# Performance work log

Measured on AMD Instinct MI355X. Metric: run time of the kernel, lower is better.

Reference implementation:

```python
import jax, jax.numpy as jnp
import numpy as np

B, S, HID = 2, 1024, 1024
NH, CH, HD = 16, 32, 64          # standard heads, constitutional heads, head_dim
TRUST = 64


def setup_inputs() -> dict:
    key = jax.random.key(0)
    ks = jax.random.split(key, 16)
    g = lambda k, sh, sc: jax.random.normal(k, sh, dtype=jnp.float32) * sc
    w = 1.0 / np.sqrt(HID)
    inp = {
        'hidden_states': g(ks[0], (B, S, HID), 1.0),
        'attention_mask': g(ks[1], (B, 1, S, S), 1.0),
        'trust_scores': jax.random.uniform(ks[2], (B, TRUST), dtype=jnp.float32),
        'Wq': g(ks[3], (HID, HID), w), 'bq': jnp.zeros((HID,), jnp.float32),
        'Wk': g(ks[4], (HID, HID), w), 'bk': jnp.zeros((HID,), jnp.float32),
        'Wv': g(ks[5], (HID, HID), w), 'bv': jnp.zeros((HID,), jnp.float32),
        'Wcq': g(ks[6], (HID, CH * HD), w), 'bcq': jnp.zeros((CH * HD,), jnp.float32),
        'Wck': g(ks[7], (HID, CH * HD), w), 'bck': jnp.zeros((CH * HD,), jnp.float32),
        'Wcv': g(ks[8], (HID, CH * HD), w), 'bcv': jnp.zeros((CH * HD,), jnp.float32),
        'Wt': g(ks[9], (TRUST, NH), 1.0 / np.sqrt(TRUST)), 'bt': jnp.zeros((NH,), jnp.float32),
        'Wo': g(ks[10], (HID, HID), w), 'bo': jnp.zeros((HID,), jnp.float32),
    }
    return inp


def reference(hidden_states, attention_mask, trust_scores,
              Wq, bq, Wk, bk, Wv, bv,
              Wcq, bcq, Wck, bck, Wcv, bcv,
              Wt, bt, Wo, bo):
    x = hidden_states
    scale = 1.0 / np.sqrt(HD).astype(np.float32)

    # standard QKV -> [B, NH, S, HD]
    q = (x @ Wq + bq).reshape(B, S, NH, HD)
    k = (x @ Wk + bk).reshape(B, S, NH, HD)
    v = (x @ Wv + bv).reshape(B, S, NH, HD)
    scores = jnp.einsum('bqhd,bkhd->bhqk', q, k) * scale  # [B,NH,S,S]
    scores = scores + attention_mask                       # additive mask

    # constitutional QKV -> [B, CH, S, HD]
    cq = (x @ Wcq + bcq).reshape(B, S, CH, HD)
    ck = (x @ Wck + bck).reshape(B, S, CH, HD)
    const_scores = jnp.einsum('bqhd,bkhd->bhqk', cq, ck) * scale  # [B,CH,S,S]

    # trust weighting: [B,TRUST] -> [B,NH] broadcast over [S,S]
    tw = trust_scores @ Wt + bt
    scores = scores * tw[:, :, None, None]

    # combine: per-head scores + mean over constitutional heads
    combined = scores + jnp.mean(const_scores, axis=1, keepdims=True)
    probs = jax.nn.softmax(combined, axis=-1)  # dropout is identity in eval

    context = jnp.einsum('bhqk,bkhd->bqhd', probs, v).reshape(B, S, HID)
    output = context @ Wo + bo
    return output, probs


if __name__ == '__main__':
    out, probs = reference(**setup_inputs())
    print(out.shape, probs.shape)
```

## Files before the change

kernel.cpp:

```cpp
#include <hip/hip_runtime.h>


typedef __bf16 bf16x8 __attribute__((ext_vector_type(8)));
typedef __bf16 bf16x4 __attribute__((ext_vector_type(4)));
typedef short  s16x4  __attribute__((ext_vector_type(4)));
typedef float  f32x4  __attribute__((ext_vector_type(4)));

static constexpr int Sq  = 1024;
static constexpr int LDP = 7168;

#if defined(__has_builtin)
#  if __has_builtin(__builtin_amdgcn_mfma_f32_16x16x16bf16_1k)
#    define HAVE_MFMA16B 1
#  endif
#endif

__device__ __forceinline__ void mfma16(f32x4& c, bf16x4 a, bf16x4 b)
{
#ifdef HAVE_MFMA16B
    union { bf16x4 h; s16x4 s; } ua, ub;
    ua.h = a; ub.h = b;
    c = __builtin_amdgcn_mfma_f32_16x16x16bf16_1k(ua.s, ub.s, c, 0, 0, 0);
#else
    asm volatile("v_mfma_f32_16x16x16_bf16 %0, %1, %2, %0"
                 : "+v"(c) : "v"(a), "v"(b));
#endif
}

template<int ROWS>
__device__ __forceinline__ void stage_g(const __bf16* g, int ld, __bf16* s, int tid)
{
    constexpr int PER = (ROWS * 4) / 256;
    int w = tid >> 6, l = tid & 63;
#pragma unroll
    for (int i = 0; i < PER; i++) {
        int bc = w * 64 + i * 256;
        int chunk = bc + l;
        int row = chunk >> 2, part = (chunk & 3) * 8;
        const __bf16* gp = g + (size_t)row * ld + part;
        __bf16* sp = s + (size_t)bc * 8;
        __builtin_amdgcn_global_load_lds(
            (__attribute__((address_space(1))) void*)(gp),
            (__attribute__((address_space(3))) void*)(sp), 16, 0, 0);
    }
}

template<int BM, int BN, int EPI>
__global__ __launch_bounds__(256) void gemm_nt(
    const __bf16* __restrict__ A, int lda,
    const __bf16* __restrict__ B, int ldb,
    void* __restrict__ Cout, int ldc,
    const float* __restrict__ bias, int Ksz, float alpha)
{
    constexpr int WM = BM / 2, WN = BN / 2, FM = WM / 16, FN = WN / 16;
    __shared__ __bf16 As[BM][32];
    __shared__ __bf16 Bs[BN][32];
    int tid = threadIdx.x;
    int w = tid >> 6, l = tid & 63;
    int wr = w >> 1, wc = w & 1;
    int lr = l & 15, kp = (l >> 4) * 8;
    int bm = blockIdx.x * BM, bn = blockIdx.y * BN;
    int z = blockIdx.z;

    size_t zA = 0, zC = 0;
    if constexpr (EPI == 2) { zA = (size_t)z * 1024 * LDP; zC = (size_t)z * Sq * Sq; }

    f32x4 acc[FM][FN];
#pragma unroll
    for (int i = 0; i < FM; i++)
#pragma unroll
        for (int j = 0; j < FN; j++) acc[i][j] = (f32x4){0.f, 0.f, 0.f, 0.f};

    for (int k0 = 0; k0 < Ksz; k0 += 32) {
        stage_g<BM>(A + zA + (size_t)bm * lda + k0, lda, &As[0][0], tid);
        stage_g<BN>(B + zA + (size_t)bn * ldb + k0, ldb, &Bs[0][0], tid);
        __syncthreads();
        bf16x8 av[FM], bv[FN];
#pragma unroll
        for (int i = 0; i < FM; i++) av[i] = *(const bf16x8*)&As[wr * WM + i * 16 + lr][kp];
#pragma unroll
        for (int j = 0; j < FN; j++) bv[j] = *(const bf16x8*)&Bs[wc * WN + j * 16 + lr][kp];
#pragma unroll
        for (int i = 0; i < FM; i++)
#pragma unroll
            for (int j = 0; j < FN; j++)
                acc[i][j] = __builtin_amdgcn_mfma_f32_16x16x32_bf16(av[i], bv[j], acc[i][j], 0, 0, 0);
        __syncthreads();
    }

    int dr = (l >> 4) * 4, dc = l & 15;
#pragma unroll
    for (int i = 0; i < FM; i++)
#pragma unroll
        for (int j = 0; j < FN; j++)
#pragma unroll
            for (int t = 0; t < 4; t++) {
                int row = bm + wr * WM + i * 16 + dr + t;
                int col = bn + wc * WN + j * 16 + dc;
                float v = acc[i][j][t];
                size_t off = zC + (size_t)row * ldc + col;
                if constexpr (EPI == 0)      ((__bf16*)Cout)[off] = (__bf16)(v + bias[col]);
                else if constexpr (EPI == 1) ((float*)Cout)[off]  = v + bias[col];
                else                         ((float*)Cout)[off]  = v * alpha;
            }
}

__global__ __launch_bounds__(256, 2) void attn_fused(
    const __bf16* __restrict__ PROJ, const __bf16* __restrict__ Kp,
    const __bf16* __restrict__ Vp,
    const float* __restrict__ mask, const float* __restrict__ CM,
    const float* __restrict__ TW, float* __restrict__ probs,
    __bf16* __restrict__ CTXb)
{
    __shared__ float ctxred[4][64][36];
    __shared__ float red[32][4];

    int tid = threadIdx.x;
    int w = tid >> 6, l = tid & 63;
    int lr = l & 15, g = l >> 4, kp = g * 8;

    int bid = blockIdx.x;
    int low3 = bid & 7;
    int t6   = bid >> 3;
    int h    = t6 & 15;
    int g64  = (t6 >> 4) * 8 + low3;
    int b    = g64 >> 5;
    int bm   = (g64 & 31) * 32;
    int z    = b * 16 + h;

    const __bf16* Qg  = PROJ + (size_t)(b * 1024 + bm) * LDP + h * 64;
    const __bf16* Kzp = Kp + (size_t)z * 65536;
    const __bf16* Vzp = Vp + (size_t)z * 65536;

    bf16x8 qv[2][2];
#pragma unroll
    for (int i = 0; i < 2; i++)
#pragma unroll
        for (int kk = 0; kk < 2; kk++)
            qv[i][kk] = *(const bf16x8*)(Qg + (size_t)(i * 16 + lr) * LDP + kk * 32 + kp);

    f32x4 acc[2][16];
#pragma unroll
    for (int i = 0; i < 2; i++)
#pragma unroll
        for (int j = 0; j < 16; j++) acc[i][j] = (f32x4){0.f, 0.f, 0.f, 0.f};

#pragma unroll
    for (int j = 0; j < 16; j++) {
        int T = w * 16 + j;
        bf16x8 k0 = *(const bf16x8*)(Kzp + ((size_t)(T * 2 + 0) * 64 + l) * 8);
        bf16x8 k1 = *(const bf16x8*)(Kzp + ((size_t)(T * 2 + 1) * 64 + l) * 8);
#pragma unroll
        for (int i = 0; i < 2; i++) {
            acc[i][j] = __builtin_amdgcn_mfma_f32_16x16x32_bf16(k0, qv[i][0], acc[i][j], 0, 0, 0);
            acc[i][j] = __builtin_amdgcn_mfma_f32_16x16x32_bf16(k1, qv[i][1], acc[i][j], 0, 0, 0);
        }
    }

    float twv = TW[z];
    float s1 = 0.125f * twv;
    const float* Mb  = mask + (size_t)b * Sq * Sq;
    const float* CMb = CM   + (size_t)b * Sq * Sq;

    float sm[2];
#pragma unroll
    for (int i = 0; i < 2; i++) {
        size_t rb = (size_t)(bm + i * 16 + lr) * 1024;
        float s = 0.f;
#pragma unroll
        for (int j = 0; j < 16; j++) {
            int off = w * 256 + j * 16 + g * 4;
            f32x4 mk = *(const f32x4*)(Mb + rb + off);
            f32x4 c4 = *(const f32x4*)(CMb + rb + off);
#pragma unroll
            for (int t = 0; t < 4; t++) {
                float e = __expf(fmaf(acc[i][j][t], s1, fmaf(mk[t], twv, c4[t])));
                acc[i][j][t] = e;
                s += e;
            }
        }
        s += __shfl_xor(s, 16);
        s += __shfl_xor(s, 32);
        sm[i] = s;
    }
    if (g == 0) { red[lr][w] = sm[0]; red[16 + lr][w] = sm[1]; }
    __syncthreads();

    float inv[2];
#pragma unroll
    for (int i = 0; i < 2; i++) {
        const float* r = red[i * 16 + lr];
        inv[i] = 1.0f / (r[0] + r[1] + r[2] + r[3]);
    }

    float* Pg = probs + (size_t)z * Sq * Sq;
    f32x4 c[2][4];
#pragma unroll
    for (int i = 0; i < 2; i++)
#pragma unroll
        for (int nt = 0; nt < 4; nt++) c[i][nt] = (f32x4){0.f, 0.f, 0.f, 0.f};

#pragma unroll
    for (int j = 0; j < 16; j++) {
        int T = w * 16 + j;
        int kb = w * 256 + j * 16 + g * 4;
        bf16x4 vb[4];
#pragma unroll
        for (int nt = 0; nt < 4; nt++)
            vb[nt] = *(const bf16x4*)(Vzp + ((size_t)(T * 4 + nt) * 64 + l) * 4);
#pragma unroll
        for (int i = 0; i < 2; i++) {
            f32x4 p;
#pragma unroll
            for (int t = 0; t < 4; t++) p[t] = acc[i][j][t] * inv[i];
            *(f32x4*)(Pg + (size_t)(bm + i * 16 + lr) * 1024 + kb) = p;
            bf16x4 pa;
#pragma unroll
            for (int t = 0; t < 4; t++) pa[t] = (__bf16)p[t];
#pragma unroll
            for (int nt = 0; nt < 4; nt++)
                mfma16(c[i][nt], pa, vb[nt]);
        }
    }

#pragma unroll
    for (int i = 0; i < 2; i++)
#pragma unroll
        for (int nt = 0; nt < 4; nt++)
            *(f32x4*)&ctxred[w][nt * 16 + lr][i * 16 + g * 4] = c[i][nt];
    __syncthreads();

    int q8 = tid & 31, dq = (tid >> 5) * 8;
    bf16x8 o;
#pragma unroll
    for (int e = 0; e < 8; e++) {
        int d = dq + e;
        float s = ctxred[0][d][q8] + ctxred[1][d][q8] + ctxred[2][d][q8] + ctxred[3][d][q8];
        o[e] = (__bf16)s;
    }
    *(bf16x8*)&CTXb[(size_t)(b * 1024 + bm + q8) * 1024 + h * 64 + dq] = o;
}

__global__ __launch_bounds__(256) void convert_f32_bf16(
    const float* __restrict__ src, __bf16* __restrict__ dst)
{
    int i = blockIdx.x * 256 + threadIdx.x;
    size_t base = (size_t)i * 8;
    float4 a = *(const float4*)(src + base);
    float4 b = *(const float4*)(src + base + 4);
    bf16x8 o;
    o[0] = (__bf16)a.x; o[1] = (__bf16)a.y; o[2] = (__bf16)a.z; o[3] = (__bf16)a.w;
    o[4] = (__bf16)b.x; o[5] = (__bf16)b.y; o[6] = (__bf16)b.z; o[7] = (__bf16)b.w;
    *(bf16x8*)(dst + base) = o;
}

__global__ __launch_bounds__(256) void transpose_all(
    const float* __restrict__ Wq, const float* __restrict__ Wk,
    const float* __restrict__ Wv, const float* __restrict__ Wcq,
    const float* __restrict__ Wck, const float* __restrict__ Wo,
    __bf16* __restrict__ Wall, __bf16* __restrict__ WoT)
{
    int zz = blockIdx.z;
    const float* src;
    int nof, ld;
    switch (zz) {
        case 0: src = Wq;  nof = 0;    ld = 1024; break;
        case 1: src = Wk;  nof = 0;    ld = 1024; break;
        case 2: src = Wv;  nof = 0;    ld = 1024; break;
        case 3: src = Wcq; nof = 0;    ld = 2048; break;
        case 4: src = Wcq; nof = 1024; ld = 2048; break;
        case 5: src = Wck; nof = 0;    ld = 2048; break;
        case 6: src = Wck; nof = 1024; ld = 2048; break;
        default: src = Wo; nof = 0;    ld = 1024; break;
    }
    __bf16* dst = (zz == 7) ? WoT : Wall + (size_t)zz * 1024 * 1024;

    __shared__ float t[32][33];
    int tx = threadIdx.x, ty = threadIdx.y;
    int n0 = blockIdx.x * 32, k0 = blockIdx.y * 32;
#pragma unroll
    for (int i = 0; i < 4; i++)
        t[ty + i * 8][tx] = src[(size_t)(k0 + ty + i * 8) * ld + nof + n0 + tx];
    __syncthreads();
#pragma unroll
    for (int i = 0; i < 4; i++)
        dst[(size_t)(n0 + ty + i * 8) * 1024 + k0 + tx] = (__bf16)t[tx][ty + i * 8];
}

__global__ __launch_bounds__(256) void pack_k(
    const __bf16* __restrict__ PROJ, __bf16* __restrict__ Kp)
{
    int z = blockIdx.y, b = z >> 4, h = z & 15;
    int t = threadIdx.x;
    int T  = blockIdx.x * 2 + (t >> 7);
    int kk = (t >> 6) & 1, g = (t >> 4) & 3, lr = t & 15;
    bf16x8 v = *(const bf16x8*)(PROJ + (size_t)(b * 1024 + T * 16 + lr) * LDP
                                + 1024 + h * 64 + kk * 32 + g * 8);
    *(bf16x8*)(Kp + (size_t)z * 65536 + ((size_t)(T * 2 + kk) * 64 + g * 16 + lr) * 8) = v;
}

__global__ __launch_bounds__(256) void pack_v(
    const __bf16* __restrict__ PROJ, __bf16* __restrict__ Vp)
{
    int z = blockIdx.y, b = z >> 4, h = z & 15;
    int T = blockIdx.x;
    int t = threadIdx.x;
    int nt = t >> 6, g = (t >> 4) & 3, lr = t & 15;
    bf16x4 v;
#pragma unroll
    for (int e = 0; e < 4; e++)
        v[e] = PROJ[(size_t)(b * 1024 + T * 16 + g * 4 + e) * LDP
                    + 2048 + h * 64 + nt * 16 + lr];
    *(bf16x4*)(Vp + (size_t)z * 65536 + ((size_t)(T * 4 + nt) * 64 + g * 16 + lr) * 4) = v;
}

__global__ void pack_bias(const float* bq, const float* bk, const float* bv,
                          const float* bcq, const float* bck, float* ball)
{
    int i = blockIdx.x * 256 + threadIdx.x;
    if (i >= LDP) return;
    float v;
    if (i < 1024) v = bq[i];
    else if (i < 2048) v = bk[i - 1024];
    else if (i < 3072) v = bv[i - 2048];
    else if (i < 5120) v = bcq[i - 3072];
    else v = bck[i - 5120];
    ball[i] = v;
}

__global__ void tw_kernel(const float* __restrict__ trust, const float* __restrict__ Wt,
                          const float* __restrict__ bt, float* __restrict__ tw)
{
    int i = threadIdx.x;
    if (i >= 32) return;
    int b = i >> 4, h = i & 15;
    float s = bt[h];
    for (int k = 0; k < 64; k++) s += trust[b * 64 + k] * Wt[k * 16 + h];
    tw[i] = s;
}

extern "C" void kernel_launch(void* const* d_in, const int* in_sizes, int n_in,
                              void* d_out, int out_size, void* d_ws, size_t ws_size,
                              hipStream_t stream)
{
    (void)in_sizes; (void)n_in; (void)out_size; (void)ws_size;
    const float* x     = (const float*)d_in[0];
    const float* mask  = (const float*)d_in[1];
    const float* trust = (const float*)d_in[2];
    const float* Wq  = (const float*)d_in[3];  const float* bq  = (const float*)d_in[4];
    const float* Wk  = (const float*)d_in[5];  const float* bk  = (const float*)d_in[6];
    const float* Wv  = (const float*)d_in[7];  const float* bv  = (const float*)d_in[8];
    const float* Wcq = (const float*)d_in[9];  const float* bcq = (const float*)d_in[10];
    const float* Wck = (const float*)d_in[11]; const float* bck = (const float*)d_in[12];
    const float* Wt  = (const float*)d_in[15]; const float* bt  = (const float*)d_in[16];
    const float* Wo  = (const float*)d_in[17]; const float* bo  = (const float*)d_in[18];

    float* out   = (float*)d_out;
    float* probs = out + (size_t)2 * Sq * 1024;

    constexpr size_t MB = 1u << 20;
    char* w8 = (char*)d_ws;
    __bf16* xb   = (__bf16*)(w8 + 0 * MB);
    __bf16* Wall = (__bf16*)(w8 + 4 * MB);
    float*  ball = (float*) (w8 + 19 * MB);
    float*  TW   = (float*) (w8 + 19 * MB + 65536);
    __bf16* WoT  = (__bf16*)(w8 + 19 * MB + 131072);
    __bf16* PROJ = (__bf16*)(w8 + 22 * MB);
    __bf16* Vp   = (__bf16*)(w8 + 50 * MB);
    float*  CM   = (float*) (w8 + 54 * MB);
    __bf16* Kp   = (__bf16*)(w8 + 62 * MB);
    __bf16* CTXb = (__bf16*)(w8 + 0 * MB);

    dim3 tb(32, 8);

    convert_f32_bf16<<<1024, 256, 0, stream>>>(x, xb);
    transpose_all<<<dim3(32, 32, 8), tb, 0, stream>>>(Wq, Wk, Wv, Wcq, Wck, Wo, Wall, WoT);
    pack_bias<<<28, 256, 0, stream>>>(bq, bk, bv, bcq, bck, ball);
    tw_kernel<<<1, 64, 0, stream>>>(trust, Wt, bt, TW);

    gemm_nt<128, 128, 0><<<dim3(16, 56, 1), 256, 0, stream>>>(
        xb, 1024, Wall, 1024, PROJ, LDP, ball, 1024, 0.f);

    pack_k<<<dim3(32, 32), 256, 0, stream>>>(PROJ, Kp);
    pack_v<<<dim3(64, 32), 256, 0, stream>>>(PROJ, Vp);

    gemm_nt<128, 64, 2><<<dim3(8, 16, 2), 256, 0, stream>>>(
        PROJ + 3072, LDP, PROJ + 5120, LDP, CM, 1024, nullptr, 2048, 0.00390625f);

    attn_fused<<<dim3(1024), 256, 0, stream>>>(PROJ, Kp, Vp, mask, CM, TW, probs, CTXb);

    gemm_nt<64, 64, 1><<<dim3(32, 16, 1), 256, 0, stream>>>(
        CTXb, 1024, WoT, 1024, out, 1024, bo, 1024, 0.f);
}
```

Before: 202.9 us.

## Fuse K/V packing into projection GEMM epilogue and use exp2 with prescaled log2e

Result: faster. 196.5 us (-3.2%).

```diff
diff --git a/kernel.cpp b/kernel.cpp
--- a/kernel.cpp
+++ b/kernel.cpp
@@ -8,6 +8,7 @@
 
 static constexpr int Sq  = 1024;
 static constexpr int LDP = 7168;
+static constexpr float LOG2E = 1.44269504f;
 
 #if defined(__has_builtin)
 #  if __has_builtin(__builtin_amdgcn_mfma_f32_16x16x16bf16_1k)
@@ -50,7 +51,8 @@
     const __bf16* __restrict__ A, int lda,
     const __bf16* __restrict__ B, int ldb,
     void* __restrict__ Cout, int ldc,
-    const float* __restrict__ bias, int Ksz, float alpha)
+    const float* __restrict__ bias, int Ksz, float alpha,
+    __bf16* __restrict__ KpOut, __bf16* __restrict__ VpOut)
 {
     constexpr int WM = BM / 2, WN = BN / 2, FM = WM / 16, FN = WN / 16;
     __shared__ __bf16 As[BM][32];
@@ -89,20 +91,74 @@
     }
 
     int dr = (l >> 4) * 4, dc = l & 15;
-#pragma unroll
-    for (int i = 0; i < FM; i++)
-#pragma unroll
-        for (int j = 0; j < FN; j++)
-#pragma unroll
-            for (int t = 0; t < 4; t++) {
-                int row = bm + wr * WM + i * 16 + dr + t;
-                int col = bn + wc * WN + j * 16 + dc;
-                float v = acc[i][j][t];
-                size_t off = zC + (size_t)row * ldc + col;
-                if constexpr (EPI == 0)      ((__bf16*)Cout)[off] = (__bf16)(v + bias[col]);
-                else if constexpr (EPI == 1) ((float*)Cout)[off]  = v + bias[col];
-                else                         ((float*)Cout)[off]  = v * alpha;
+
+    if constexpr (EPI == 0) {
+        if (bn >= 1024 && bn < 2048) {
+#pragma unroll
+            for (int i = 0; i < FM; i++) {
+                int r0 = bm + wr * WM + i * 16 + dr;
+                int bb = r0 >> 10, T = (r0 & 1023) >> 4;
+#pragma unroll
+                for (int j = 0; j < FN; j++) {
+                    int c  = bn + wc * WN + j * 16 + dc;
+                    int d  = c - 1024;
+                    int hh = d >> 6, dd = d & 63;
+                    int kk2 = dd >> 5, gg = (dd & 31) >> 3, ee = dd & 7;
+                    size_t kbase = (size_t)(bb * 16 + hh) * 65536
+                                 + ((size_t)(T * 2 + kk2) * 64 + gg * 16) * 8 + ee;
+                    float bcol = bias[c];
+#pragma unroll
+                    for (int t = 0; t < 4; t++)
+                        KpOut[kbase + (size_t)(dr + t) * 8] = (__bf16)(acc[i][j][t] + bcol);
+                }
             }
+        } else if (bn >= 2048 && bn < 3072) {
+#pragma unroll
+            for (int i = 0; i < FM; i++) {
+                int r0 = bm + wr * WM + i * 16 + dr;
+                int bb = r0 >> 10, rl = r0 & 1023;
+                int T = rl >> 4, gq = (rl & 15) >> 2;
+#pragma unroll
+                for (int j = 0; j < FN; j++) {
+                    int c  = bn + wc * WN + j * 16 + dc;
+                    int d  = c - 2048;
+                    int hh = d >> 6, nt = (d & 63) >> 4, lrr = d & 15;
+                    float bcol = bias[c];
+                    bf16x4 q;
+#pragma unroll
+                    for (int t = 0; t < 4; t++) q[t] = (__bf16)(acc[i][j][t] + bcol);
+                    *(bf16x4*)(VpOut + (size_t)(bb * 16 + hh) * 65536
+                               + ((size_t)(T * 4 + nt) * 64 + gq * 16 + lrr) * 4) = q;
+                }
+            }
+        } else {
+#pragma unroll
+            for (int i = 0; i < FM; i++)
+#pragma unroll
+                for (int j = 0; j < FN; j++)
+#pragma unroll
+                    for (int t = 0; t < 4; t++) {
+                        int row = bm + wr * WM + i * 16 + dr + t;
+                        int col = bn + wc * WN + j * 16 + dc;
+                        ((__bf16*)Cout)[(size_t)row * ldc + col] =
+                            (__bf16)(acc[i][j][t] + bias[col]);
+                    }
+        }
+    } else {
+#pragma unroll
+        for (int i = 0; i < FM; i++)
+#pragma unroll
+            for (int j = 0; j < FN; j++)
+#pragma unroll
+                for (int t = 0; t < 4; t++) {
+                    int row = bm + wr * WM + i * 16 + dr + t;
+                    int col = bn + wc * WN + j * 16 + dc;
+                    float v = acc[i][j][t];
+                    size_t off = zC + (size_t)row * ldc + col;
+                    if constexpr (EPI == 1) ((float*)Cout)[off] = v + bias[col];
+                    else                    ((float*)Cout)[off] = v * alpha;
+                }
+    }
 }
 
 __global__ __launch_bounds__(256, 2) void attn_fused(
@@ -174,7 +230,7 @@
             f32x4 c4 = *(const f32x4*)(CMb + rb + off);
 #pragma unroll
             for (int t = 0; t < 4; t++) {
-                float e = __expf(fmaf(acc[i][j][t], s1, fmaf(mk[t], twv, c4[t])));
+                float e = __builtin_amdgcn_exp2f(fmaf(acc[i][j][t], s1, fmaf(mk[t], twv, c4[t])));
                 acc[i][j][t] = e;
                 s += e;
             }
@@ -287,56 +343,27 @@
         dst[(size_t)(n0 + ty + i * 8) * 1024 + k0 + tx] = (__bf16)t[tx][ty + i * 8];
 }
 
-__global__ __launch_bounds__(256) void pack_k(
-    const __bf16* __restrict__ PROJ, __bf16* __restrict__ Kp)
-{
-    int z = blockIdx.y, b = z >> 4, h = z & 15;
-    int t = threadIdx.x;
-    int T  = blockIdx.x * 2 + (t >> 7);
-    int kk = (t >> 6) & 1, g = (t >> 4) & 3, lr = t & 15;
-    bf16x8 v = *(const bf16x8*)(PROJ + (size_t)(b * 1024 + T * 16 + lr) * LDP
-                                + 1024 + h * 64 + kk * 32 + g * 8);
-    *(bf16x8*)(Kp + (size_t)z * 65536 + ((size_t)(T * 2 + kk) * 64 + g * 16 + lr) * 8) = v;
-}
-
-__global__ __launch_bounds__(256) void pack_v(
-    const __bf16* __restrict__ PROJ, __bf16* __restrict__ Vp)
-{
-    int z = blockIdx.y, b = z >> 4, h = z & 15;
-    int T = blockIdx.x;
-    int t = threadIdx.x;
-    int nt = t >> 6, g = (t >> 4) & 3, lr = t & 15;
-    bf16x4 v;
-#pragma unroll
-    for (int e = 0; e < 4; e++)
-        v[e] = PROJ[(size_t)(b * 1024 + T * 16 + g * 4 + e) * LDP
-                    + 2048 + h * 64 + nt * 16 + lr];
-    *(bf16x4*)(Vp + (size_t)z * 65536 + ((size_t)(T * 4 + nt) * 64 + g * 16 + lr) * 4) = v;
-}
-
-__global__ void pack_bias(const float* bq, const float* bk, const float* bv,
-                          const float* bcq, const float* bck, float* ball)
+__global__ void small_prep(const float* bq, const float* bk, const float* bv,
+                           const float* bcq, const float* bck,
+                           const float* trust, const float* Wt, const float* bt,
+                           float* ball, float* tw)
 {
     int i = blockIdx.x * 256 + threadIdx.x;
-    if (i >= LDP) return;
-    float v;
-    if (i < 1024) v = bq[i];
-    else if (i < 2048) v = bk[i - 1024];
-    else if (i < 3072) v = bv[i - 2048];
-    else if (i < 5120) v = bcq[i - 3072];
-    else v = bck[i - 5120];
-    ball[i] = v;
-}
-
-__global__ void tw_kernel(const float* __restrict__ trust, const float* __restrict__ Wt,
-                          const float* __restrict__ bt, float* __restrict__ tw)
-{
-    int i = threadIdx.x;
-    if (i >= 32) return;
-    int b = i >> 4, h = i & 15;
-    float s = bt[h];
-    for (int k = 0; k < 64; k++) s += trust[b * 64 + k] * Wt[k * 16 + h];
-    tw[i] = s;
+    if (i < LDP) {
+        float v;
+        if (i < 1024) v = bq[i];
+        else if (i < 2048) v = bk[i - 1024];
+        else if (i < 3072) v = bv[i - 2048];
+        else if (i < 5120) v = bcq[i - 3072];
+        else v = bck[i - 5120];
+        ball[i] = v;
+    } else if (blockIdx.x == 28 && threadIdx.x < 32) {
+        int j = threadIdx.x;
+        int b = j >> 4, h = j & 15;
+        float s = bt[h];
+        for (int k = 0; k < 64; k++) s += trust[b * 64 + k] * Wt[k * 16 + h];
+        tw[j] = s * LOG2E;
+    }
 }
 
 extern "C" void kernel_launch(void* const* d_in, const int* in_sizes, int n_in,
@@ -375,20 +402,17 @@
 
     convert_f32_bf16<<<1024, 256, 0, stream>>>(x, xb);
     transpose_all<<<dim3(32, 32, 8), tb, 0, stream>>>(Wq, Wk, Wv, Wcq, Wck, Wo, Wall, WoT);
-    pack_bias<<<28, 256, 0, stream>>>(bq, bk, bv, bcq, bck, ball);
-    tw_kernel<<<1, 64, 0, stream>>>(trust, Wt, bt, TW);
+    small_prep<<<29, 256, 0, stream>>>(bq, bk, bv, bcq, bck, trust, Wt, bt, ball, TW);
 
     gemm_nt<128, 128, 0><<<dim3(16, 56, 1), 256, 0, stream>>>(
-        xb, 1024, Wall, 1024, PROJ, LDP, ball, 1024, 0.f);
-
-    pack_k<<<dim3(32, 32), 256, 0, stream>>>(PROJ, Kp);
-    pack_v<<<dim3(64, 32), 256, 0, stream>>>(PROJ, Vp);
+        xb, 1024, Wall, 1024, PROJ, LDP, ball, 1024, 0.f, Kp, Vp);
 
     gemm_nt<128, 64, 2><<<dim3(8, 16, 2), 256, 0, stream>>>(
-        PROJ + 3072, LDP, PROJ + 5120, LDP, CM, 1024, nullptr, 2048, 0.00390625f);
+        PROJ + 3072, LDP, PROJ + 5120, LDP, CM, 1024, nullptr, 2048,
+        0.00390625f * LOG2E, nullptr, nullptr);
 
     attn_fused<<<dim3(1024), 256, 0, stream>>>(PROJ, Kp, Vp, mask, CM, TW, probs, CTXb);
 
     gemm_nt<64, 64, 1><<<dim3(32, 16, 1), 256, 0, stream>>>(
-        CTXb, 1024, WoT, 1024, out, 1024, bo, 1024, 0.f);
-}
+        CTXb, 1024, WoT, 1024, out, 1024, bo, 1024, 0.f, nullptr, nullptr);
+}
```
